# Optimization experiments

Hardware: AMD Instinct MI355X
Metric: run time of the kernel (lower is better)

Reference implementation:

```python
import jax, jax.numpy as jnp
import numpy as np

TEMPERATURE = 0.1
NUM_RISK_GROUPS = 4
SIM_WEIGHT = 1.0
CONTRAST_WEIGHT = 0.1
NEG = jnp.float32(-1e9)  # finite stand-in for -inf (grad-safe, exp() == 0 in fp32)


def setup_inputs() -> dict:
    key = jax.random.key(0)
    k1, k2, k3, k4 = jax.random.split(key, 4)
    N, D = 8192, 256
    return {
        "log_risks": jax.random.normal(k1, (N,), dtype=jnp.float32),
        "times": jax.random.uniform(k2, (N,), dtype=jnp.float32),
        "censor": jnp.ones((N,), dtype=jnp.int32),
        "wsi_embeddings": jax.random.normal(k3, (N, D), dtype=jnp.float32),
        "omic_embeddings": jax.random.normal(k4, (N, D), dtype=jnp.float32),
    }


def _cox_loss(log_risks, times, censor):
    lr = jnp.clip(log_risks, -10.0, 10.0)
    order = jnp.argsort(-times)  # descending times
    slr = lr[order]
    sc = censor[order]
    # at-risk sum for index i is sum_{j<=i} exp(slr_j) (arange <= i mask) -> cumsum
    at_risk = jnp.cumsum(jnp.exp(slr))
    li = slr - jnp.log(at_risk + 1e-15)
    mask = (sc == 1)
    cnt = jnp.maximum(jnp.sum(mask), 1)
    return -jnp.sum(jnp.where(mask, li, 0.0)) / cnt


def _similarity_loss(a, b):
    na = jnp.maximum(jnp.linalg.norm(a, axis=1), 1e-8)
    nb = jnp.maximum(jnp.linalg.norm(b, axis=1), 1e-8)
    cos = jnp.clip(jnp.sum(a * b, axis=1) / (na * nb), -1.0, 1.0)
    return jnp.mean(1.0 - cos)


def _contrastive_loss(emb, times):
    # NOTE: assumes censor == 1 for all samples (as in setup_inputs), so the
    # uncensored subset is the whole batch and shapes stay static.
    G = NUM_RISK_GROUPS
    q = jnp.quantile(times, jnp.linspace(0.0, 1.0, G + 1))
    # group = #thresholds q[1..G] that t >= ; max bucket clipped to G-1
    groups = jnp.clip(jnp.sum(times[:, None] >= q[None, 1:], axis=1), 0, G - 1)
    z = emb / jnp.maximum(jnp.linalg.norm(emb, axis=1, keepdims=True), 1e-12)
    sim = (z @ z.T) / TEMPERATURE  # [N, N]
    N = emb.shape[0]
    eye = jnp.eye(N, dtype=bool)
    same = groups[:, None] == groups[None, :]
    pos = same & ~eye
    offdiag = ~eye  # pos | neg == all off-diagonal entries
    lse_pos = jax.nn.logsumexp(jnp.where(pos, sim, NEG), axis=1)
    lse_all = jax.nn.logsumexp(jnp.where(offdiag, sim, NEG), axis=1)
    neg_any = jnp.any(~same & ~eye, axis=1)
    valid = jnp.any(pos, axis=1) & neg_any
    loss = -lse_pos + lse_all
    cnt = jnp.maximum(jnp.sum(valid), 1)
    return jnp.sum(jnp.where(valid, loss, 0.0)) / cnt


def reference(log_risks, times, censor, wsi_embeddings, omic_embeddings):
    cox = _cox_loss(log_risks, times, censor)
    sim = _similarity_loss(wsi_embeddings, omic_embeddings)
    c_wsi = _contrastive_loss(wsi_embeddings, times)
    c_omic = _contrastive_loss(omic_embeddings, times)
    contrast = (c_wsi + c_omic) / 2.0
    return cox + SIM_WEIGHT * sim + CONTRAST_WEIGHT * contrast
```

## Files before the change

### kernel.cpp

```cpp
#include <hip/hip_runtime.h>


#define NN 8192
#define DD 256

typedef __attribute__((ext_vector_type(4))) float f32x4;
typedef __attribute__((ext_vector_type(4))) int i32x4;
typedef __attribute__((ext_vector_type(2))) long l64x2;

__device__ inline void gl_lds16(const void* g, void* l) {
  __builtin_amdgcn_global_load_lds(
      (const __attribute__((address_space(1))) unsigned int*)g,
      (__attribute__((address_space(3))) unsigned int*)l, 16, 0, 0);
}

__global__ void __launch_bounds__(256) k_rows(
    const float* __restrict__ lr, const float* __restrict__ times,
    const int* __restrict__ censor,
    const float* __restrict__ wsi, const float* __restrict__ omic,
    unsigned char* __restrict__ pw, unsigned char* __restrict__ po,
    float* __restrict__ pslots, float* __restrict__ gsum) {
  __shared__ __align__(16) float st[1024];
  __shared__ __align__(16) float se[1024];
  __shared__ float red[4][3];
  const int tid = threadIdx.x;
  const int lane = tid & 63;
  const int wv = tid >> 6;
  const int i = blockIdx.x * 4 + wv;

  if (blockIdx.x < 64) {
    ((f32x4*)gsum)[blockIdx.x * 256 + tid] = (f32x4){0.f, 0.f, 0.f, 0.f};
  }

  const float4 w = ((const float4*)(wsi + (size_t)i * DD))[lane];
  const float4 o = ((const float4*)(omic + (size_t)i * DD))[lane];
  float nw = w.x * w.x + w.y * w.y + w.z * w.z + w.w * w.w;
  float no = o.x * o.x + o.y * o.y + o.z * o.z + o.w * o.w;
  float dd = w.x * o.x + w.y * o.y + w.z * o.z + w.w * o.w;
  for (int m = 1; m < 64; m <<= 1) {
    nw += __shfl_xor(nw, m);
    no += __shfl_xor(no, m);
    dd += __shfl_xor(dd, m);
  }
  const float nws = sqrtf(nw), nos = sqrtf(no);

  const float ti = times[i];
  int rk = 0;
  float ar = 0.f;
  for (int c = 0; c < 8; ++c) {
    __syncthreads();
    for (int p = tid; p < 1024; p += 256) {
      float t = times[c * 1024 + p];
      float l = lr[c * 1024 + p];
      st[p] = t;
      se[p] = __expf(fminf(fmaxf(l, -10.f), 10.f));
    }
    __syncthreads();
#pragma unroll 4
    for (int jt = 0; jt < 16; ++jt) {
      const int p = jt * 64 + lane;
      const float t = st[p];
      const float e = se[p];
      const bool c1 = (t < ti) || ((t == ti) && ((c * 1024 + p) < i));
      rk += c1 ? 1 : 0;
      ar += c1 ? 0.f : e;
    }
  }
  for (int m = 1; m < 64; m <<= 1) {
    rk += __shfl_xor(rk, m);
    ar += __shfl_xor(ar, m);
  }

  if (lane == 0) {
    float c = dd / (fmaxf(nws, 1e-8f) * fmaxf(nos, 1e-8f));
    c = fminf(fmaxf(c, -1.f), 1.f);
    float l = fminf(fmaxf(lr[i], -10.f), 10.f);
    float li = l - logf(ar + 1e-15f);
    bool cen = (censor[i] == 1);
    red[wv][0] = cen ? li : 0.f;
    red[wv][1] = cen ? 1.f : 0.f;
    red[wv][2] = 1.f - c;
  }

  const int r = rk;
  const float iw = 1.f / fmaxf(nws, 1e-12f);
  const float io = 1.f / fmaxf(nos, 1e-12f);
  int zw = __builtin_amdgcn_cvt_pk_fp8_f32(w.x * iw, w.y * iw, 0, false);
  zw = __builtin_amdgcn_cvt_pk_fp8_f32(w.z * iw, w.w * iw, zw, true);
  int zo = __builtin_amdgcn_cvt_pk_fp8_f32(o.x * io, o.y * io, 0, false);
  zo = __builtin_amdgcn_cvt_pk_fp8_f32(o.z * io, o.w * io, zo, true);
  const size_t off = ((size_t)((lane >> 4) * 4 + ((lane >> 1) & 3)) * NN + r) * 16
                     + ((lane >> 3) & 1) * 8 + (lane & 1) * 4;
  *(unsigned int*)(pw + off) = (unsigned int)zw;
  *(unsigned int*)(po + off) = (unsigned int)zo;
  __syncthreads();
  if (tid < 3) {
    pslots[blockIdx.x * 4 + tid] =
        red[0][tid] + red[1][tid] + red[2][tid] + red[3][tid];
  }
}

__global__ void __launch_bounds__(256, 4) k_contrast(
    const unsigned char* __restrict__ pw, const unsigned char* __restrict__ po,
    float* __restrict__ gsum) {
  __shared__ __align__(16) unsigned char sbuf[2][16384];
  const int tid = threadIdx.x;
  const int lane = tid & 63;
  const int wv = tid >> 6;
  const int lo = lane & 15, q = lane >> 4;
  const int cb = blockIdx.x, rb = blockIdx.y, mz = blockIdx.z;
  const unsigned char* __restrict__ pk = (mz == 0) ? pw : po;
  const int rowbase = rb * 128 + wv * 32;
  const int colstart = cb * 512;
  const int g = cb >> 2;

  i32x4 afrag[2][4];
#pragma unroll
  for (int rt = 0; rt < 2; ++rt) {
    const size_t row = rowbase + rt * 16 + lo;
#pragma unroll
    for (int kp = 0; kp < 4; ++kp)
      afrag[rt][kp] = *(const i32x4*)(pk + ((size_t)(kp * 4 + q) * NN + row) * 16);
  }

  const unsigned char* gsrc[4];
#pragma unroll
  for (int p = 0; p < 4; ++p) {
    const int u = (wv * 4 + p) * 64 + lane;
    gsrc[p] = pk + ((size_t)(((u >> 6) & 3) * 4 + ((u >> 4) & 3)) * NN
                    + colstart + (u >> 8) * 16 + (u & 15)) * 16;
  }
  unsigned char* const ldb = &sbuf[0][(size_t)wv * 4096];

#pragma unroll
  for (int p = 0; p < 4; ++p) gl_lds16(gsrc[p], ldb + p * 1024);
  __syncthreads();

  float s[2][4] = {{0.f}};
  const int dctbase = (wv & 1) * 2;

#pragma unroll 1
  for (int st = 0; st < 8; ++st) {
    if (st < 7) {
      const size_t adv = (size_t)(st + 1) * 1024;
      const size_t bofs = ((st + 1) & 1) ? 16384 : 0;
#pragma unroll
      for (int p = 0; p < 4; ++p) gl_lds16(gsrc[p] + adv, ldb + bofs + p * 1024);
    }
    const unsigned char* buf = &sbuf[st & 1][0];
    const bool diagw = ((rowbase >> 6) == ((colstart + st * 64) >> 6));
#pragma unroll
    for (int ct = 0; ct < 4; ++ct) {
      f32x4 a0 = {0.f, 0.f, 0.f, 0.f}, a1 = {0.f, 0.f, 0.f, 0.f};
#pragma unroll
      for (int kh = 0; kh < 2; ++kh) {
        l64x2 b0 = __builtin_bit_cast(l64x2,
            *(const i32x4*)&buf[(ct * 4 + kh * 2 + 0) * 1024 + lane * 16]);
        l64x2 b1 = __builtin_bit_cast(l64x2,
            *(const i32x4*)&buf[(ct * 4 + kh * 2 + 1) * 1024 + lane * 16]);
        l64x2 x0 = __builtin_bit_cast(l64x2, afrag[0][kh * 2 + 0]);
        l64x2 x1 = __builtin_bit_cast(l64x2, afrag[0][kh * 2 + 1]);
        l64x2 y0 = __builtin_bit_cast(l64x2, afrag[1][kh * 2 + 0]);
        l64x2 y1 = __builtin_bit_cast(l64x2, afrag[1][kh * 2 + 1]);
        a0 = __builtin_amdgcn_mfma_f32_16x16x32_fp8_fp8(x0[0], b0[0], a0, 0, 0, 0);
        a1 = __builtin_amdgcn_mfma_f32_16x16x32_fp8_fp8(y0[0], b0[0], a1, 0, 0, 0);
        a0 = __builtin_amdgcn_mfma_f32_16x16x32_fp8_fp8(x0[1], b0[1], a0, 0, 0, 0);
        a1 = __builtin_amdgcn_mfma_f32_16x16x32_fp8_fp8(y0[1], b0[1], a1, 0, 0, 0);
        a0 = __builtin_amdgcn_mfma_f32_16x16x32_fp8_fp8(x1[0], b1[0], a0, 0, 0, 0);
        a1 = __builtin_amdgcn_mfma_f32_16x16x32_fp8_fp8(y1[0], b1[0], a1, 0, 0, 0);
        a0 = __builtin_amdgcn_mfma_f32_16x16x32_fp8_fp8(x1[1], b1[1], a0, 0, 0, 0);
        a1 = __builtin_amdgcn_mfma_f32_16x16x32_fp8_fp8(y1[1], b1[1], a1, 0, 0, 0);
      }
      if (diagw) {
#pragma unroll
        for (int r = 0; r < 4; ++r) {
          float e0 = __expf(fmaf(a0[r], 10.f, -10.f));
          float e1 = __expf(fmaf(a1[r], 10.f, -10.f));
          if (ct == dctbase + 0 && lo == q * 4 + r) e0 = 0.f;
          if (ct == dctbase + 1 && lo == q * 4 + r) e1 = 0.f;
          s[0][r] += e0;
          s[1][r] += e1;
        }
      } else {
#pragma unroll
        for (int r = 0; r < 4; ++r) {
          s[0][r] += __expf(fmaf(a0[r], 10.f, -10.f));
          s[1][r] += __expf(fmaf(a1[r], 10.f, -10.f));
        }
      }
    }
    __syncthreads();
  }

#pragma unroll
  for (int rt = 0; rt < 2; ++rt)
#pragma unroll
    for (int r = 0; r < 4; ++r) {
      float v = s[rt][r];
      v += __shfl_xor(v, 1); v += __shfl_xor(v, 2);
      v += __shfl_xor(v, 4); v += __shfl_xor(v, 8);
      if (lo == 0) {
        const int row = rowbase + rt * 16 + q * 4 + r;
        atomicAdd(&gsum[((size_t)mz * NN + row) * 4 + g], v);
      }
    }
}

__global__ void __launch_bounds__(1024) k_finale(
    const float* __restrict__ pslots, const float* __restrict__ gsum,
    float* __restrict__ out) {
  __shared__ float rsum[16][4];
  const int tid = threadIdx.x;
  const int lane = tid & 63, wv = tid >> 6;
  float cox = 0.f, cnt = 0.f, sim = 0.f, con = 0.f;
  for (int b = tid; b < 2048; b += 1024) {
    const float4 v = ((const float4*)pslots)[b];
    cox += v.x; cnt += v.y; sim += v.z;
  }
  for (int idx = tid; idx < 2 * NN; idx += 1024) {
    const float4 v = ((const float4*)gsum)[idx];
    const int row = idx & (NN - 1);
    const int gg = row >> 11;
    const float sg = (gg == 0) ? v.x : (gg == 1) ? v.y : (gg == 2) ? v.z : v.w;
    con += logf(v.x + v.y + v.z + v.w) - logf(sg);
  }
  for (int m = 1; m < 64; m <<= 1) {
    cox += __shfl_xor(cox, m);
    cnt += __shfl_xor(cnt, m);
    sim += __shfl_xor(sim, m);
    con += __shfl_xor(con, m);
  }
  if (lane == 0) {
    rsum[wv][0] = cox; rsum[wv][1] = cnt; rsum[wv][2] = sim; rsum[wv][3] = con;
  }
  __syncthreads();
  if (tid == 0) {
    float c0 = 0.f, c1 = 0.f, c2 = 0.f, c3 = 0.f;
    for (int k = 0; k < 16; ++k) {
      c0 += rsum[k][0]; c1 += rsum[k][1]; c2 += rsum[k][2]; c3 += rsum[k][3];
    }
    out[0] = -c0 / fmaxf(c1, 1.f) + c2 / (float)NN
             + 0.1f * 0.5f * c3 / (float)NN;
  }
}

extern "C" void kernel_launch(void* const* d_in, const int* in_sizes, int n_in,
                              void* d_out, int out_size, void* d_ws, size_t ws_size,
                              hipStream_t stream) {
  const float* lr = (const float*)d_in[0];
  const float* times = (const float*)d_in[1];
  const int* censor = (const int*)d_in[2];
  const float* wsi = (const float*)d_in[3];
  const float* omic = (const float*)d_in[4];
  float* out = (float*)d_out;

  char* ws = (char*)d_ws;
  float* pslots = (float*)ws;
  float* gsum = (float*)(ws + 32768);
  unsigned char* pw = (unsigned char*)(ws + 294912);
  unsigned char* po = (unsigned char*)(ws + 294912 + 2097152);

  k_rows<<<2048, 256, 0, stream>>>(lr, times, censor, wsi, omic, pw, po, pslots, gsum);
  k_contrast<<<dim3(16, 64, 2), 256, 0, stream>>>(pw, po, gsum);
  k_finale<<<1, 1024, 0, stream>>>(pslots, gsum, out);
}
```

Before: 157.0 us.

## Switch contrast GEMM to scaled 16x16x128 FP8 MFMA with repacked layout

Replaces the eight 16x16x32 FP8 MFMAs per k-block with two MX-scaled 16x16x128 f8f6f4 MFMAs using unit scales. The packed FP8 embedding layout is rebuilt so each lane holds 32 contiguous bytes, and the A fragments, LDS staging addresses and prefetch stride are changed to match. It also replaces __expf with a direct exp2 intrinsic on a prescaled argument, which saves a multiply per element. The aim is fewer MFMA issues and less exp overhead in the N×N similarity pass. The risk is that the new layout or operand ordering does not match what the instruction expects.

```diff
diff --git a/kernel.cpp b/kernel.cpp
--- a/kernel.cpp
+++ b/kernel.cpp
@@ -6,7 +6,7 @@
 
 typedef __attribute__((ext_vector_type(4))) float f32x4;
 typedef __attribute__((ext_vector_type(4))) int i32x4;
-typedef __attribute__((ext_vector_type(2))) long l64x2;
+typedef __attribute__((ext_vector_type(8))) int i32x8;
 
 __device__ inline void gl_lds16(const void* g, void* l) {
   __builtin_amdgcn_global_load_lds(
@@ -89,8 +89,8 @@
   zw = __builtin_amdgcn_cvt_pk_fp8_f32(w.z * iw, w.w * iw, zw, true);
   int zo = __builtin_amdgcn_cvt_pk_fp8_f32(o.x * io, o.y * io, 0, false);
   zo = __builtin_amdgcn_cvt_pk_fp8_f32(o.z * io, o.w * io, zo, true);
-  const size_t off = ((size_t)((lane >> 4) * 4 + ((lane >> 1) & 3)) * NN + r) * 16
-                     + ((lane >> 3) & 1) * 8 + (lane & 1) * 4;
+  const size_t off = ((size_t)((lane >> 5) * 4 + ((lane >> 3) & 3)) * NN + r) * 32
+                     + (lane & 7) * 4;
   *(unsigned int*)(pw + off) = (unsigned int)zw;
   *(unsigned int*)(po + off) = (unsigned int)zo;
   __syncthreads();
@@ -114,21 +114,23 @@
   const int colstart = cb * 512;
   const int g = cb >> 2;
 
-  i32x4 afrag[2][4];
+  i32x8 afrag[2][2];
 #pragma unroll
   for (int rt = 0; rt < 2; ++rt) {
     const size_t row = rowbase + rt * 16 + lo;
 #pragma unroll
-    for (int kp = 0; kp < 4; ++kp)
-      afrag[rt][kp] = *(const i32x4*)(pk + ((size_t)(kp * 4 + q) * NN + row) * 16);
+    for (int ks = 0; ks < 2; ++ks)
+      afrag[rt][ks] = *(const i32x8*)(pk + ((size_t)(ks * 4 + q) * NN + row) * 32);
   }
 
   const unsigned char* gsrc[4];
 #pragma unroll
   for (int p = 0; p < 4; ++p) {
     const int u = (wv * 4 + p) * 64 + lane;
-    gsrc[p] = pk + ((size_t)(((u >> 6) & 3) * 4 + ((u >> 4) & 3)) * NN
-                    + colstart + (u >> 8) * 16 + (u & 15)) * 16;
+    const int uct = u >> 8, uks = (u >> 7) & 1, uh = (u >> 6) & 1;
+    const int ul = u & 63;
+    gsrc[p] = pk + ((size_t)(uks * 4 + (ul >> 4)) * NN
+                    + colstart + uct * 16 + (ul & 15)) * 32 + uh * 16;
   }
   unsigned char* const ldb = &sbuf[0][(size_t)wv * 4096];
 
@@ -142,7 +144,7 @@
 #pragma unroll 1
   for (int st = 0; st < 8; ++st) {
     if (st < 7) {
-      const size_t adv = (size_t)(st + 1) * 1024;
+      const size_t adv = (size_t)(st + 1) * 2048;
       const size_t bofs = ((st + 1) & 1) ? 16384 : 0;
 #pragma unroll
       for (int p = 0; p < 4; ++p) gl_lds16(gsrc[p] + adv, ldb + bofs + p * 1024);
@@ -153,29 +155,21 @@
     for (int ct = 0; ct < 4; ++ct) {
       f32x4 a0 = {0.f, 0.f, 0.f, 0.f}, a1 = {0.f, 0.f, 0.f, 0.f};
 #pragma unroll
-      for (int kh = 0; kh < 2; ++kh) {
-        l64x2 b0 = __builtin_bit_cast(l64x2,
-            *(const i32x4*)&buf[(ct * 4 + kh * 2 + 0) * 1024 + lane * 16]);
-        l64x2 b1 = __builtin_bit_cast(l64x2,
-            *(const i32x4*)&buf[(ct * 4 + kh * 2 + 1) * 1024 + lane * 16]);
-        l64x2 x0 = __builtin_bit_cast(l64x2, afrag[0][kh * 2 + 0]);
-        l64x2 x1 = __builtin_bit_cast(l64x2, afrag[0][kh * 2 + 1]);
-        l64x2 y0 = __builtin_bit_cast(l64x2, afrag[1][kh * 2 + 0]);
-        l64x2 y1 = __builtin_bit_cast(l64x2, afrag[1][kh * 2 + 1]);
-        a0 = __builtin_amdgcn_mfma_f32_16x16x32_fp8_fp8(x0[0], b0[0], a0, 0, 0, 0);
-        a1 = __builtin_amdgcn_mfma_f32_16x16x32_fp8_fp8(y0[0], b0[0], a1, 0, 0, 0);
-        a0 = __builtin_amdgcn_mfma_f32_16x16x32_fp8_fp8(x0[1], b0[1], a0, 0, 0, 0);
-        a1 = __builtin_amdgcn_mfma_f32_16x16x32_fp8_fp8(y0[1], b0[1], a1, 0, 0, 0);
-        a0 = __builtin_amdgcn_mfma_f32_16x16x32_fp8_fp8(x1[0], b1[0], a0, 0, 0, 0);
-        a1 = __builtin_amdgcn_mfma_f32_16x16x32_fp8_fp8(y1[0], b1[0], a1, 0, 0, 0);
-        a0 = __builtin_amdgcn_mfma_f32_16x16x32_fp8_fp8(x1[1], b1[1], a0, 0, 0, 0);
-        a1 = __builtin_amdgcn_mfma_f32_16x16x32_fp8_fp8(y1[1], b1[1], a1, 0, 0, 0);
+      for (int ks = 0; ks < 2; ++ks) {
+        const int rbase = ((ct * 2 + ks) * 2) * 1024 + lane * 16;
+        i32x4 blo = *(const i32x4*)&buf[rbase];
+        i32x4 bhi = *(const i32x4*)&buf[rbase + 1024];
+        i32x8 b = __builtin_shufflevector(blo, bhi, 0, 1, 2, 3, 4, 5, 6, 7);
+        a0 = __builtin_amdgcn_mfma_scale_f32_16x16x128_f8f6f4(
+            afrag[0][ks], b, a0, 0, 0, 0, 0x7F, 0, 0x7F);
+        a1 = __builtin_amdgcn_mfma_scale_f32_16x16x128_f8f6f4(
+            afrag[1][ks], b, a1, 0, 0, 0, 0x7F, 0, 0x7F);
       }
       if (diagw) {
 #pragma unroll
         for (int r = 0; r < 4; ++r) {
-          float e0 = __expf(fmaf(a0[r], 10.f, -10.f));
-          float e1 = __expf(fmaf(a1[r], 10.f, -10.f));
+          float e0 = __builtin_amdgcn_exp2f(fmaf(a0[r], 14.4269504f, -14.4269504f));
+          float e1 = __builtin_amdgcn_exp2f(fmaf(a1[r], 14.4269504f, -14.4269504f));
           if (ct == dctbase + 0 && lo == q * 4 + r) e0 = 0.f;
           if (ct == dctbase + 1 && lo == q * 4 + r) e1 = 0.f;
           s[0][r] += e0;
@@ -184,8 +178,8 @@
       } else {
 #pragma unroll
         for (int r = 0; r < 4; ++r) {
-          s[0][r] += __expf(fmaf(a0[r], 10.f, -10.f));
-          s[1][r] += __expf(fmaf(a1[r], 10.f, -10.f));
+          s[0][r] += __builtin_amdgcn_exp2f(fmaf(a0[r], 14.4269504f, -14.4269504f));
+          s[1][r] += __builtin_amdgcn_exp2f(fmaf(a1[r], 14.4269504f, -14.4269504f));
         }
       }
     }
```

Result: faster. 146.0 us (-7.0%).
